# Kernel optimization log

Hardware: AMD Instinct MI355X
Metric: run time of the kernel (lower is better)

Reference implementation:

```python
import jax, jax.numpy as jnp
import numpy as np

N = 50000
DIM = 512
HID = 256
NCLS = 2
E = 800000


def gcn_conv(x, W, b, src, dst, deg_inv_sqrt, num_nodes):
    # GCNConv (PyG default): h = D^{-1/2} (A + I) D^{-1/2} x W + b
    h = x @ W  # [N, out]
    norm = deg_inv_sqrt[src] * deg_inv_sqrt[dst]  # [E+N]
    msgs = norm[:, None] * h[src]  # gather per edge
    out = jax.ops.segment_sum(msgs, dst, num_segments=num_nodes)
    return out + b


def setup_inputs() -> dict:
    key = jax.random.key(0)
    k1, k2, k3, k4 = jax.random.split(key, 4)
    x = jax.random.normal(k1, (N, DIM), dtype=jnp.float32)
    edge_index = jax.random.randint(k2, (2, E), 0, N, dtype=jnp.int64)
    # Glorot-style init for weights, zero bias (as PyG GCNConv)
    W1 = jax.random.normal(k3, (DIM, HID), dtype=jnp.float32) * (1.0 / np.sqrt(DIM))
    b1 = jnp.zeros((HID,), dtype=jnp.float32)
    W2 = jax.random.normal(k4, (HID, NCLS), dtype=jnp.float32) * (1.0 / np.sqrt(HID))
    b2 = jnp.zeros((NCLS,), dtype=jnp.float32)
    return {"x": x, "W1": W1, "b1": b1, "W2": W2, "b2": b2, "edge_index": edge_index}


def reference(x, W1, b1, W2, b2, edge_index):
    num_nodes = x.shape[0]
    loops = jnp.arange(num_nodes, dtype=edge_index.dtype)
    src = jnp.concatenate([edge_index[0], loops])
    dst = jnp.concatenate([edge_index[1], loops])
    # symmetric normalization with self-loops (edge_weight = 1)
    deg = jax.ops.segment_sum(jnp.ones_like(dst, dtype=x.dtype), dst, num_segments=num_nodes)
    deg_inv_sqrt = jnp.where(deg > 0, jax.lax.rsqrt(deg), 0.0)

    h = gcn_conv(x, W1, b1, src, dst, deg_inv_sqrt, num_nodes)
    h = jax.nn.relu(h)
    # dropout p=0.5 is identity at inference (training=False)
    out = gcn_conv(h, W2, b2, src, dst, deg_inv_sqrt, num_nodes)
    return out
```

## Files before the change

### kernel.cpp

```cpp
#include <hip/hip_runtime.h>
#include <stdint.h>

#define NN   50000
#define DIMK 512
#define HIDN 256
#define NE   800000

#define SCAN_ITEMS 4
#define SCAN_BLK 256
#define SCAN_PER_BLOCK (SCAN_ITEMS * SCAN_BLK)
#define NBLK ((NN + SCAN_PER_BLOCK - 1) / SCAN_PER_BLOCK)

typedef float f32x4 __attribute__((ext_vector_type(4)));
typedef short s16x8 __attribute__((ext_vector_type(8)));

static __device__ __forceinline__ unsigned short f2bf(float f) {
  union { float f; uint32_t u; } v; v.f = f;
  uint32_t u = v.u;
  u += 0x7fffu + ((u >> 16) & 1u);
  return (unsigned short)(u >> 16);
}

__global__ void k_hist(const int* __restrict__ edst, int* __restrict__ cnt) {
  int e = blockIdx.x * 256 + threadIdx.x;
  if (e < NE) atomicAdd(&cnt[edst[e]], 1);
}

__global__ __launch_bounds__(256) void k_blocksum(const int* __restrict__ cnt,
                                                  int* __restrict__ blocksum) {
  const int t = threadIdx.x;
  const int base = blockIdx.x * SCAN_PER_BLOCK + t * SCAN_ITEMS;
  int s = 0;
#pragma unroll
  for (int j = 0; j < SCAN_ITEMS; ++j) { int i = base + j; if (i < NN) s += cnt[i]; }
#pragma unroll
  for (int o = 1; o < 64; o <<= 1) s += __shfl_xor(s, o);
  __shared__ int wsum[4];
  if ((t & 63) == 0) wsum[t >> 6] = s;
  __syncthreads();
  if (t == 0) blocksum[blockIdx.x] = wsum[0] + wsum[1] + wsum[2] + wsum[3];
}

__global__ void k_scanblocks(const int* __restrict__ blocksum, int* __restrict__ blockoff) {
  const int t = threadIdx.x;
  int own = (t < NBLK) ? blocksum[t] : 0;
  int v = own;
#pragma unroll
  for (int o = 1; o < 64; o <<= 1) { int u = __shfl_up(v, o); if (t >= o) v += u; }
  if (t < NBLK) blockoff[t] = v - own;
}

__global__ __launch_bounds__(256) void k_finalize(const int* __restrict__ cnt,
                                                  const int* __restrict__ blockoff,
                                                  int* __restrict__ offsets,
                                                  int* __restrict__ cursor,
                                                  float* __restrict__ dis) {
  const int t = threadIdx.x;
  const int l = t & 63, w = t >> 6;
  const int base = blockIdx.x * SCAN_PER_BLOCK + t * SCAN_ITEMS;
  int c[SCAN_ITEMS]; int s = 0;
#pragma unroll
  for (int j = 0; j < SCAN_ITEMS; ++j) { int i = base + j; c[j] = (i < NN) ? cnt[i] : 0; s += c[j]; }
  const int own = s;
#pragma unroll
  for (int o = 1; o < 64; o <<= 1) { int u = __shfl_up(s, o); if (l >= o) s += u; }
  __shared__ int wt[4];
  if (l == 63) wt[w] = s;
  __syncthreads();
  int waveoff = 0;
  for (int ww = 0; ww < w; ++ww) waveoff += wt[ww];
  int run = blockoff[blockIdx.x] + waveoff + (s - own);
#pragma unroll
  for (int j = 0; j < SCAN_ITEMS; ++j) {
    int i = base + j;
    if (i < NN) {
      offsets[i] = run;
      cursor[i]  = run;
      dis[i] = rsqrtf((float)(c[j] + 1));
      run += c[j];
    }
  }
  if (blockIdx.x == 0 && t == 0) offsets[NN] = NE;
}

__global__ void k_scatter(const int* __restrict__ esrc, const int* __restrict__ edst,
                          int* __restrict__ cursor, int* __restrict__ ssorted) {
  int e = blockIdx.x * 256 + threadIdx.x;
  if (e < NE) {
    int d = edst[e];
    int p = atomicAdd(&cursor[d], 1);
    ssorted[p] = esrc[e];
  }
}

__global__ void k_prep_w1t(const float* __restrict__ W1, char* __restrict__ w1t) {
  int tid = blockIdx.x * 256 + threadIdx.x;
  int c  = tid & 255;
  int k  = tid >> 8;
  int tt = k >> 5;
  int kk = k & 31;
  int g  = kk >> 3;
  int i  = kk & 7;
  unsigned short v = f2bf(W1[k * HIDN + c]);
  int byte = tt * 16384 + c * 64 + ((g ^ ((c >> 1) & 3)) << 4) + i * 2;
  *(unsigned short*)(w1t + byte) = v;
}

__global__ __launch_bounds__(256) void k_gemm1(const float* __restrict__ x,
                                               const char* __restrict__ w1t,
                                               const float* __restrict__ dis,
                                               unsigned short* __restrict__ h1s) {
  __shared__ char lds[32768];
  const int tid = threadIdx.x;
  const int l = tid & 63;
  const int r = l & 15;
  const int g = l >> 4;
  const int rowbase = blockIdx.x * 64 + (tid >> 6) * 16;
  int arow = rowbase + r;
  if (arow >= NN) arow = NN - 1;

  const char* gb = w1t + tid * 16;

  s16x8 Rb[4];
  float4 Ra0, Ra1;
  {
#pragma unroll
    for (int i = 0; i < 4; ++i)
      Rb[i] = *(const s16x8*)(gb + i * 4096);
    const float4* ap = (const float4*)(x + (size_t)arow * DIMK + g * 8);
    Ra0 = ap[0]; Ra1 = ap[1];
  }

  f32x4 acc[16];
#pragma unroll
  for (int j = 0; j < 16; ++j) acc[j] = (f32x4){0.f, 0.f, 0.f, 0.f};

  int cur = 0;
  for (int t = 0; t < 16; ++t) {
#pragma unroll
    for (int i = 0; i < 4; ++i)
      *(s16x8*)(lds + cur * 16384 + i * 4096 + tid * 16) = Rb[i];
    __syncthreads();

    const int tn = (t + 1 < 16) ? (t + 1) : 15;
    s16x8 nRb[4];
#pragma unroll
    for (int i = 0; i < 4; ++i)
      nRb[i] = *(const s16x8*)(gb + tn * 16384 + i * 4096);
    const float4* ap = (const float4*)(x + (size_t)arow * DIMK + tn * 32 + g * 8);
    float4 na0 = ap[0], na1 = ap[1];

    s16x8 af;
    af[0] = (short)f2bf(Ra0.x); af[1] = (short)f2bf(Ra0.y);
    af[2] = (short)f2bf(Ra0.z); af[3] = (short)f2bf(Ra0.w);
    af[4] = (short)f2bf(Ra1.x); af[5] = (short)f2bf(Ra1.y);
    af[6] = (short)f2bf(Ra1.z); af[7] = (short)f2bf(Ra1.w);

#pragma unroll
    for (int j = 0; j < 16; ++j) {
      const int c = j * 16 + r;
      const s16x8 bf = *(const s16x8*)(lds + cur * 16384 + c * 64 +
                                       ((g ^ ((c >> 1) & 3)) << 4));
      acc[j] = __builtin_amdgcn_mfma_f32_16x16x32_bf16(af, bf, acc[j], 0, 0, 0);
    }

#pragma unroll
    for (int i = 0; i < 4; ++i) Rb[i] = nRb[i];
    Ra0 = na0; Ra1 = na1;
    cur ^= 1;
  }

  int orow[4]; float dsv[4];
#pragma unroll
  for (int rr = 0; rr < 4; ++rr) {
    orow[rr] = rowbase + 4 * g + rr;
    dsv[rr] = (orow[rr] < NN) ? dis[orow[rr]] : 0.f;
  }
#pragma unroll
  for (int j = 0; j < 16; ++j) {
#pragma unroll
    for (int rr = 0; rr < 4; ++rr) {
      if (orow[rr] < NN)
        h1s[(size_t)orow[rr] * HIDN + j * 16 + r] = f2bf(acc[j][rr] * dsv[rr]);
    }
  }
}

__global__ __launch_bounds__(256) void k_agg1(const unsigned short* __restrict__ h1s,
                                              const int* __restrict__ offsets,
                                              const int* __restrict__ ssorted,
                                              const float* __restrict__ dis,
                                              const float* __restrict__ b1,
                                              const float* __restrict__ W2,
                                              float* __restrict__ h2s) {
  const int w = threadIdx.x >> 6;
  const int l = threadIdx.x & 63;
  const int d = blockIdx.x * 4 + w;
  if (d >= NN) return;

  float a0, a1, a2, a3;
  {
    uint2 v = *(const uint2*)(h1s + (size_t)d * HIDN + l * 4);
    a0 = __uint_as_float(v.x << 16);
    a1 = __uint_as_float(v.x & 0xffff0000u);
    a2 = __uint_as_float(v.y << 16);
    a3 = __uint_as_float(v.y & 0xffff0000u);
  }
  const int off0 = offsets[d], off1 = offsets[d + 1];
  int e = off0;
  for (; e + 4 <= off1; e += 4) {
    int s0 = ssorted[e], s1 = ssorted[e + 1], s2 = ssorted[e + 2], s3 = ssorted[e + 3];
    uint2 v0 = *(const uint2*)(h1s + (size_t)s0 * HIDN + l * 4);
    uint2 v1 = *(const uint2*)(h1s + (size_t)s1 * HIDN + l * 4);
    uint2 v2 = *(const uint2*)(h1s + (size_t)s2 * HIDN + l * 4);
    uint2 v3 = *(const uint2*)(h1s + (size_t)s3 * HIDN + l * 4);
    a0 += __uint_as_float(v0.x << 16) + __uint_as_float(v1.x << 16) +
          __uint_as_float(v2.x << 16) + __uint_as_float(v3.x << 16);
    a1 += __uint_as_float(v0.x & 0xffff0000u) + __uint_as_float(v1.x & 0xffff0000u) +
          __uint_as_float(v2.x & 0xffff0000u) + __uint_as_float(v3.x & 0xffff0000u);
    a2 += __uint_as_float(v0.y << 16) + __uint_as_float(v1.y << 16) +
          __uint_as_float(v2.y << 16) + __uint_as_float(v3.y << 16);
    a3 += __uint_as_float(v0.y & 0xffff0000u) + __uint_as_float(v1.y & 0xffff0000u) +
          __uint_as_float(v2.y & 0xffff0000u) + __uint_as_float(v3.y & 0xffff0000u);
  }
  for (; e < off1; ++e) {
    int s = ssorted[e];
    uint2 v = *(const uint2*)(h1s + (size_t)s * HIDN + l * 4);
    a0 += __uint_as_float(v.x << 16);
    a1 += __uint_as_float(v.x & 0xffff0000u);
    a2 += __uint_as_float(v.y << 16);
    a3 += __uint_as_float(v.y & 0xffff0000u);
  }

  const float dsd = dis[d];
  const int c0 = l * 4;
  float r0 = fmaxf(a0 * dsd + b1[c0 + 0], 0.f);
  float r1 = fmaxf(a1 * dsd + b1[c0 + 1], 0.f);
  float r2 = fmaxf(a2 * dsd + b1[c0 + 2], 0.f);
  float r3 = fmaxf(a3 * dsd + b1[c0 + 3], 0.f);

  float p0 = r0 * W2[(c0 + 0) * 2] + r1 * W2[(c0 + 1) * 2] +
             r2 * W2[(c0 + 2) * 2] + r3 * W2[(c0 + 3) * 2];
  float p1 = r0 * W2[(c0 + 0) * 2 + 1] + r1 * W2[(c0 + 1) * 2 + 1] +
             r2 * W2[(c0 + 2) * 2 + 1] + r3 * W2[(c0 + 3) * 2 + 1];
#pragma unroll
  for (int o = 1; o < 64; o <<= 1) {
    p0 += __shfl_xor(p0, o);
    p1 += __shfl_xor(p1, o);
  }
  if (l == 0) {
    h2s[(size_t)d * 2 + 0] = dsd * p0;
    h2s[(size_t)d * 2 + 1] = dsd * p1;
  }
}

__global__ void k_agg2(const float* __restrict__ h2s, const int* __restrict__ offsets,
                       const int* __restrict__ ssorted, const float* __restrict__ dis,
                       const float* __restrict__ b2, float* __restrict__ out) {
  int d = blockIdx.x * 256 + threadIdx.x;
  if (d >= NN) return;
  float2 sv = *(const float2*)(h2s + (size_t)d * 2);
  float a0 = sv.x, a1 = sv.y;
  int off0 = offsets[d], off1 = offsets[d + 1];
  int e = off0;
  for (; e + 4 <= off1; e += 4) {
    int s0 = ssorted[e], s1 = ssorted[e + 1], s2 = ssorted[e + 2], s3 = ssorted[e + 3];
    float2 v0 = *(const float2*)(h2s + (size_t)s0 * 2);
    float2 v1 = *(const float2*)(h2s + (size_t)s1 * 2);
    float2 v2 = *(const float2*)(h2s + (size_t)s2 * 2);
    float2 v3 = *(const float2*)(h2s + (size_t)s3 * 2);
    a0 += v0.x + v1.x + v2.x + v3.x;
    a1 += v0.y + v1.y + v2.y + v3.y;
  }
  for (; e < off1; ++e) {
    int s = ssorted[e];
    float2 v = *(const float2*)(h2s + (size_t)s * 2);
    a0 += v.x; a1 += v.y;
  }
  float dsd = dis[d];
  out[(size_t)d * 2 + 0] = dsd * a0 + b2[0];
  out[(size_t)d * 2 + 1] = dsd * a1 + b2[1];
}

extern "C" void kernel_launch(void* const* d_in, const int* in_sizes, int n_in,
                              void* d_out, int out_size, void* d_ws, size_t ws_size,
                              hipStream_t stream) {
  (void)in_sizes; (void)n_in; (void)out_size; (void)ws_size;
  const float* x   = (const float*)d_in[0];
  const float* W1  = (const float*)d_in[1];
  const float* b1  = (const float*)d_in[2];
  const float* W2  = (const float*)d_in[3];
  const float* b2  = (const float*)d_in[4];
  const int*   ei  = (const int*)d_in[5];
  const int* esrc = ei;
  const int* edst = ei + NE;
  float* out = (float*)d_out;

  char* ws = (char*)d_ws;
  unsigned short* h1s = (unsigned short*)(ws + 0);
  char*  w1t     = ws + 25600000;
  float* dis     = (float*)(ws + 25862144);
  float* h2s     = (float*)(ws + 26062144);
  int*   cnt     = (int*)(ws + 26462144);
  int*   offsets = (int*)(ws + 26662144);
  int*   cursor  = (int*)(ws + 26862208);
  int*   ssorted = (int*)(ws + 27062208);
  int*   blocksum= (int*)(ws + 30262208);
  int*   blockoff= (int*)(ws + 30262464);

  hipMemsetAsync(cnt, 0, NN * sizeof(int), stream);
  k_hist<<<(NE + 255) / 256, 256, 0, stream>>>(edst, cnt);
  k_blocksum<<<NBLK, 256, 0, stream>>>(cnt, blocksum);
  k_scanblocks<<<1, 64, 0, stream>>>(blocksum, blockoff);
  k_finalize<<<NBLK, 256, 0, stream>>>(cnt, blockoff, offsets, cursor, dis);
  k_scatter<<<(NE + 255) / 256, 256, 0, stream>>>(esrc, edst, cursor, ssorted);
  k_prep_w1t<<<(DIMK * HIDN) / 256, 256, 0, stream>>>(W1, w1t);
  k_gemm1<<<(NN + 63) / 64, 256, 0, stream>>>(x, w1t, dis, h1s);
  k_agg1<<<(NN + 3) / 4, 256, 0, stream>>>(h1s, offsets, ssorted, dis, b1, W2, h2s);
  k_agg2<<<(NN + 255) / 256, 256, 0, stream>>>(h2s, offsets, ssorted, dis, b2, out);
}
```

Measured before the change: 222.1 us.

## Rewrite GEMM1 with 32x32x16 MFMA, per-wave 32-row tiles, no LDS

The first-layer GEMM now has each wave compute a 32-row by 256-column tile with 32x32x16 bf16 MFMAs. B fragments are read straight from a repacked global W1 layout, double-buffered in registers, instead of being staged through LDS with block barriers. The A rows are prefetched four steps ahead and converted with packed bf16 conversion instructions. The aim is to remove LDS traffic and syncthreads and to cut conversion cost. In exchange each wave keeps a large register footprint (128 accumulators plus buffers), which limits occupancy, and W1 is re-read from L2 by every wave.

```diff
diff --git a/kernel.cpp b/kernel.cpp
--- a/kernel.cpp
+++ b/kernel.cpp
@@ -11,14 +11,21 @@
 #define SCAN_PER_BLOCK (SCAN_ITEMS * SCAN_BLK)
 #define NBLK ((NN + SCAN_PER_BLOCK - 1) / SCAN_PER_BLOCK)
 
-typedef float f32x4 __attribute__((ext_vector_type(4)));
-typedef short s16x8 __attribute__((ext_vector_type(8)));
+typedef float f32x4  __attribute__((ext_vector_type(4)));
+typedef float f32x16 __attribute__((ext_vector_type(16)));
+typedef short s16x8  __attribute__((ext_vector_type(8)));
 
 static __device__ __forceinline__ unsigned short f2bf(float f) {
   union { float f; uint32_t u; } v; v.f = f;
   uint32_t u = v.u;
   u += 0x7fffu + ((u >> 16) & 1u);
   return (unsigned short)(u >> 16);
+}
+
+static __device__ __forceinline__ uint32_t cvt_pk_bf16(float lo, float hi) {
+  uint32_t r;
+  asm("v_cvt_pk_bf16_f32 %0, %1, %2" : "=v"(r) : "v"(lo), "v"(hi));
+  return r;
 }
 
 __global__ void k_hist(const int* __restrict__ edst, int* __restrict__ cnt) {
@@ -97,91 +104,91 @@
   int tid = blockIdx.x * 256 + threadIdx.x;
   int c  = tid & 255;
   int k  = tid >> 8;
-  int tt = k >> 5;
-  int kk = k & 31;
+  int t  = k >> 4;
+  int kk = k & 15;
   int g  = kk >> 3;
   int i  = kk & 7;
+  int j  = c >> 5;
+  int cc = c & 31;
   unsigned short v = f2bf(W1[k * HIDN + c]);
-  int byte = tt * 16384 + c * 64 + ((g ^ ((c >> 1) & 3)) << 4) + i * 2;
-  *(unsigned short*)(w1t + byte) = v;
-}
-
-__global__ __launch_bounds__(256) void k_gemm1(const float* __restrict__ x,
-                                               const char* __restrict__ w1t,
-                                               const float* __restrict__ dis,
-                                               unsigned short* __restrict__ h1s) {
-  __shared__ char lds[32768];
-  const int tid = threadIdx.x;
-  const int l = tid & 63;
-  const int r = l & 15;
-  const int g = l >> 4;
-  const int rowbase = blockIdx.x * 64 + (tid >> 6) * 16;
-  int arow = rowbase + r;
-  if (arow >= NN) arow = NN - 1;
-
-  const char* gb = w1t + tid * 16;
-
-  s16x8 Rb[4];
-  float4 Ra0, Ra1;
-  {
-#pragma unroll
-    for (int i = 0; i < 4; ++i)
-      Rb[i] = *(const s16x8*)(gb + i * 4096);
-    const float4* ap = (const float4*)(x + (size_t)arow * DIMK + g * 8);
-    Ra0 = ap[0]; Ra1 = ap[1];
-  }
-
-  f32x4 acc[16];
-#pragma unroll
-  for (int j = 0; j < 16; ++j) acc[j] = (f32x4){0.f, 0.f, 0.f, 0.f};
-
-  int cur = 0;
-  for (int t = 0; t < 16; ++t) {
-#pragma unroll
-    for (int i = 0; i < 4; ++i)
-      *(s16x8*)(lds + cur * 16384 + i * 4096 + tid * 16) = Rb[i];
-    __syncthreads();
-
-    const int tn = (t + 1 < 16) ? (t + 1) : 15;
-    s16x8 nRb[4];
-#pragma unroll
-    for (int i = 0; i < 4; ++i)
-      nRb[i] = *(const s16x8*)(gb + tn * 16384 + i * 4096);
-    const float4* ap = (const float4*)(x + (size_t)arow * DIMK + tn * 32 + g * 8);
-    float4 na0 = ap[0], na1 = ap[1];
-
-    s16x8 af;
-    af[0] = (short)f2bf(Ra0.x); af[1] = (short)f2bf(Ra0.y);
-    af[2] = (short)f2bf(Ra0.z); af[3] = (short)f2bf(Ra0.w);
-    af[4] = (short)f2bf(Ra1.x); af[5] = (short)f2bf(Ra1.y);
-    af[6] = (short)f2bf(Ra1.z); af[7] = (short)f2bf(Ra1.w);
-
-#pragma unroll
-    for (int j = 0; j < 16; ++j) {
-      const int c = j * 16 + r;
-      const s16x8 bf = *(const s16x8*)(lds + cur * 16384 + c * 64 +
-                                       ((g ^ ((c >> 1) & 3)) << 4));
-      acc[j] = __builtin_amdgcn_mfma_f32_16x16x32_bf16(af, bf, acc[j], 0, 0, 0);
-    }
-
-#pragma unroll
-    for (int i = 0; i < 4; ++i) Rb[i] = nRb[i];
-    Ra0 = na0; Ra1 = na1;
-    cur ^= 1;
-  }
-
-  int orow[4]; float dsv[4];
-#pragma unroll
-  for (int rr = 0; rr < 4; ++rr) {
-    orow[rr] = rowbase + 4 * g + rr;
-    dsv[rr] = (orow[rr] < NN) ? dis[orow[rr]] : 0.f;
-  }
-#pragma unroll
-  for (int j = 0; j < 16; ++j) {
-#pragma unroll
-    for (int rr = 0; rr < 4; ++rr) {
-      if (orow[rr] < NN)
-        h1s[(size_t)orow[rr] * HIDN + j * 16 + r] = f2bf(acc[j][rr] * dsv[rr]);
+  *(unsigned short*)(w1t + (t * 8 + j) * 1024 + (g * 32 + cc) * 16 + i * 2) = v;
+}
+
+#define GSTEP(T, AC, BC)                                                        \
+  {                                                                             \
+    union { s16x8 v; uint32_t u[4]; } AF;                                       \
+    AF.u[0] = cvt_pk_bf16(AC[0].x, AC[0].y);                                    \
+    AF.u[1] = cvt_pk_bf16(AC[0].z, AC[0].w);                                    \
+    AF.u[2] = cvt_pk_bf16(AC[1].x, AC[1].y);                                    \
+    AF.u[3] = cvt_pk_bf16(AC[1].z, AC[1].w);                                    \
+    _Pragma("unroll")                                                           \
+    for (int j = 0; j < 8; ++j)                                                 \
+      acc[j] = __builtin_amdgcn_mfma_f32_32x32x16_bf16(AF.v, BC[j], acc[j], 0, 0, 0); \
+    if ((T) + 2 < 32) {                                                         \
+      _Pragma("unroll")                                                         \
+      for (int j = 0; j < 8; ++j)                                               \
+        BC[j] = *(const s16x8*)(wb + ((T) + 2) * 8192 + j * 1024);              \
+    }                                                                           \
+    if ((T) + 4 < 32) {                                                         \
+      AC[0] = ap[((T) + 4) * 4];                                                \
+      AC[1] = ap[((T) + 4) * 4 + 1];                                            \
+    }                                                                           \
+  }
+
+__global__ __launch_bounds__(256, 2) void k_gemm1(const float* __restrict__ x,
+                                                  const char* __restrict__ w1t,
+                                                  const float* __restrict__ dis,
+                                                  unsigned short* __restrict__ h1s) {
+  const int l = threadIdx.x & 63;
+  const int wid = (blockIdx.x * 256 + threadIdx.x) >> 6;
+  const int R0 = wid * 32;
+  if (R0 >= NN) return;
+  const int h = l >> 5;
+  int ra = R0 + (l & 31);
+  if (ra >= NN) ra = NN - 1;
+
+  const float4* ap = (const float4*)(x + (size_t)ra * DIMK) + h * 2;
+  const char* wb = w1t + l * 16;
+
+  f32x16 acc[8];
+#pragma unroll
+  for (int j = 0; j < 8; ++j)
+#pragma unroll
+    for (int g = 0; g < 16; ++g) acc[j][g] = 0.f;
+
+  float4 A0[2], A1[2], A2[2], A3[2];
+  A0[0] = ap[0];  A0[1] = ap[1];
+  A1[0] = ap[4];  A1[1] = ap[5];
+  A2[0] = ap[8];  A2[1] = ap[9];
+  A3[0] = ap[12]; A3[1] = ap[13];
+  s16x8 Ba[8], Bb[8];
+#pragma unroll
+  for (int j = 0; j < 8; ++j) Ba[j] = *(const s16x8*)(wb + j * 1024);
+#pragma unroll
+  for (int j = 0; j < 8; ++j) Bb[j] = *(const s16x8*)(wb + 8192 + j * 1024);
+
+#pragma unroll
+  for (int q = 0; q < 8; ++q) {
+    GSTEP(4 * q + 0, A0, Ba);
+    GSTEP(4 * q + 1, A1, Bb);
+    GSTEP(4 * q + 2, A2, Ba);
+    GSTEP(4 * q + 3, A3, Bb);
+  }
+
+  const int cc = l & 31;
+  float dv[16];
+#pragma unroll
+  for (int g = 0; g < 16; ++g) {
+    int row = R0 + (g & 3) + 8 * (g >> 2) + 4 * h;
+    dv[g] = (row < NN) ? dis[row] : 0.f;
+  }
+#pragma unroll
+  for (int j = 0; j < 8; ++j) {
+#pragma unroll
+    for (int g = 0; g < 16; ++g) {
+      int row = R0 + (g & 3) + 8 * (g >> 2) + 4 * h;
+      if (row < NN)
+        h1s[(size_t)row * HIDN + j * 32 + cc] = f2bf(acc[j][g] * dv[g]);
     }
   }
 }
@@ -315,7 +322,11 @@
   k_finalize<<<NBLK, 256, 0, stream>>>(cnt, blockoff, offsets, cursor, dis);
   k_scatter<<<(NE + 255) / 256, 256, 0, stream>>>(esrc, edst, cursor, ssorted);
   k_prep_w1t<<<(DIMK * HIDN) / 256, 256, 0, stream>>>(W1, w1t);
-  k_gemm1<<<(NN + 63) / 64, 256, 0, stream>>>(x, w1t, dis, h1s);
+  {
+    const int nwaves = (NN + 31) / 32;
+    const int nblk   = (nwaves + 3) / 4;
+    k_gemm1<<<nblk, 256, 0, stream>>>(x, w1t, dis, h1s);
+  }
   k_agg1<<<(NN + 3) / 4, 256, 0, stream>>>(h1s, offsets, ssorted, dis, b1, W2, h2s);
   k_agg2<<<(NN + 255) / 256, 256, 0, stream>>>(h2s, offsets, ssorted, dis, b2, out);
 }
```

After: 220.6 us. No clear change (-0.7%).
